# Optimization experiments

Hardware: AMD Instinct MI355X
Metric: run time of the kernel (lower is better)

## Reference

```python
import jax, jax.numpy as jnp
import numpy as np

B, N, E, H = 8, 1500, 3000, 256
HOPS = 3


def setup_inputs() -> dict:
    key = jax.random.key(0)
    ks = jax.random.split(key, 9)
    node_state = jax.random.normal(ks[0], (B, N, H), jnp.float32)
    edge_vec = jax.random.normal(ks[1], (B, E, H), jnp.float32)
    # sparse-ish 0/1 incidence matrices (avg ~3 nonzeros per row)
    node2edge = (jax.random.uniform(ks[2], (B, E, N)) < 0.002).astype(jnp.float32)
    edge2node = (jax.random.uniform(ks[3], (B, N, E)) < 0.002).astype(jnp.float32)
    s = 1.0 / np.sqrt(H).astype(np.float32)
    W_max = jax.random.uniform(ks[4], (H, H), jnp.float32, -s, s)        # linear_max, no bias
    W_fz = jax.random.uniform(ks[5], (4 * H, H), jnp.float32, -s, s)     # gated fusion
    b_fz = jnp.zeros((H,), jnp.float32)
    W_z = jax.random.uniform(ks[6], (2 * H, H), jnp.float32, -s, s)      # GRU gates, no bias
    W_r = jax.random.uniform(ks[7], (2 * H, H), jnp.float32, -s, s)
    W_t = jax.random.uniform(ks[8], (2 * H, H), jnp.float32, -s, s)
    return dict(node_state=node_state, edge_vec=edge_vec, node2edge=node2edge,
                edge2node=edge2node, W_max=W_max, W_fz=W_fz, b_fz=b_fz,
                W_z=W_z, W_r=W_r, W_t=W_t)


def _msg_pass(node_state, edge_vec, n2e, e2n):
    # n2e: (B,E,N), e2n: (B,N,E)
    edge_emb = jnp.einsum('ben,bnh->beh', n2e, node_state) + edge_vec   # (B,E,H)
    norm = jnp.sum(e2n, axis=2, keepdims=True) + 1.0                     # self-loop degree norm
    return (jnp.einsum('bne,beh->bnh', e2n, edge_emb) + node_state) / norm


def _gated_fusion(h, x, W_fz, b_fz):
    z = jax.nn.sigmoid(jnp.concatenate([h, x, h * x, h - x], -1) @ W_fz + b_fz)
    return (1.0 - z) * h + z * x


def _gru_step(h, x, W_z, W_r, W_t):
    hx = jnp.concatenate([h, x], -1)
    z = jax.nn.sigmoid(hx @ W_z)
    r = jax.nn.sigmoid(hx @ W_r)
    t = jnp.tanh(jnp.concatenate([r * h, x], -1) @ W_t)
    return (1.0 - z) * h + z * t


def reference(node_state, edge_vec, node2edge, edge2node, W_max, W_fz, b_fz, W_z, W_r, W_t):
    n2e_T = jnp.swapaxes(node2edge, 1, 2)   # (B,N,E)
    e2n_T = jnp.swapaxes(edge2node, 1, 2)   # (B,E,N)
    for _ in range(HOPS):
        bw = _msg_pass(node_state, edge_vec, node2edge, edge2node)
        fw = _msg_pass(node_state, edge_vec, e2n_T, n2e_T)
        agg = _gated_fusion(fw, bw, W_fz, b_fz)
        node_state = _gru_step(node_state, agg, W_z, W_r, W_t)
    # graph max pool: linear then max over nodes
    graph_embedding = jnp.max(node_state @ W_max, axis=1)[None]  # (1,B,H)
    return jnp.swapaxes(node_state, 0, 1), graph_embedding       # (N,B,H), (1,B,H)
```

## Files before the change

kernel.cpp:

```cpp
#include <hip/hip_runtime.h>
#include <hip/hip_bf16.h>
#include <stdint.h>

#define Bb 8
#define Nn 1500
#define Ee 3000
#define Hh 256
#define NHOPS 3
#define CAP 32
#define Mrows (Bb*Nn)
#define BE (Bb*Ee)
#define BN (Bb*Nn)

typedef __bf16 bf16x8 __attribute__((ext_vector_type(8)));
typedef float f32x4 __attribute__((ext_vector_type(4)));

__device__ __forceinline__ float sigmoidf_(float x){ return 1.f/(1.f+__expf(-x)); }

__device__ __forceinline__ unsigned short f2b(float f){
  union { float f; unsigned int u; } x; x.f = f;
  unsigned int r = (x.u + 0x7fffu + ((x.u >> 16) & 1u)) >> 16;
  return (unsigned short)r;
}
__device__ __forceinline__ float b2f(unsigned short u){
  union { unsigned int u; float f; } x; x.u = ((unsigned int)u) << 16;
  return x.f;
}
__device__ __forceinline__ ushort4 pack4(float4 v){
  return make_ushort4(f2b(v.x), f2b(v.y), f2b(v.z), f2b(v.w));
}
__device__ __forceinline__ float4 unpack4(ushort4 u){
  return make_float4(b2f(u.x), b2f(u.y), b2f(u.z), b2f(u.w));
}

#define GLL16(g, l) __builtin_amdgcn_global_load_lds( \
    (const __attribute__((address_space(1))) unsigned int*)(g), \
    (__attribute__((address_space(3))) unsigned int*)(l), 16, 0, 0)

__device__ __forceinline__ void rowscan_body(const float* __restrict__ mat, int R, int C,
                                             int* __restrict__ rowIdx, int* __restrict__ rowCnt,
                                             int* __restrict__ colIdx, int* __restrict__ colCnt,
                                             int blk) {
  int w = __builtin_amdgcn_readfirstlane((int)(threadIdx.x >> 6));
  int g = blk * 4 + w;
  if (g >= Bb * R) return;
  int b = g / R;
  int lane = threadIdx.x & 63;
  const float4* base = (const float4*)(mat + (size_t)g * C);
  int nq = C >> 2;
  int cnt = 0;
  for (int q0 = 0; q0 < nq; q0 += 64) {
    int q = q0 + lane;
    float4 v = make_float4(0.f, 0.f, 0.f, 0.f);
    if (q < nq) v = base[q];
    unsigned long long m0 = __ballot(v.x != 0.f);
    unsigned long long m1 = __ballot(v.y != 0.f);
    unsigned long long m2 = __ballot(v.z != 0.f);
    unsigned long long m3 = __ballot(v.w != 0.f);
    unsigned long long below = (1ull << lane) - 1ull;
    int myc = cnt + __popcll(m0 & below) + __popcll(m1 & below)
                  + __popcll(m2 & below) + __popcll(m3 & below);
    int c = q * 4;
    #pragma unroll
    for (int j = 0; j < 4; ++j) {
      float vv = (j == 0) ? v.x : (j == 1) ? v.y : (j == 2) ? v.z : v.w;
      if (vv != 0.f) {
        if (myc < CAP) rowIdx[(size_t)g * CAP + myc] = c + j;
        int slot = atomicAdd(&colCnt[b * C + c + j], 1);
        if (slot < CAP) colIdx[(size_t)(b * C + c + j) * CAP + slot] = g - b * R;
        ++myc;
      }
    }
    cnt += __popcll(m0) + __popcll(m1) + __popcll(m2) + __popcll(m3);
  }
  if (lane == 0) rowCnt[g] = cnt;
}

__global__ void preprocess_kernel(const float* __restrict__ n2e, const float* __restrict__ e2n,
                                  int* __restrict__ Aidx, int* __restrict__ cntA,
                                  int* __restrict__ Didx, int* __restrict__ cntD,
                                  int* __restrict__ Bidx, int* __restrict__ cntB,
                                  int* __restrict__ Cidx, int* __restrict__ cntC,
                                  const float* __restrict__ Wfz, const float* __restrict__ Wz,
                                  const float* __restrict__ Wr, const float* __restrict__ Wt,
                                  const float* __restrict__ Wmax,
                                  unsigned short* __restrict__ WfzT, unsigned short* __restrict__ WzrT,
                                  unsigned short* __restrict__ WtT, unsigned short* __restrict__ WmaxT,
                                  const float* __restrict__ in_ns, float* __restrict__ ns,
                                  const float* __restrict__ in_ev, unsigned short* __restrict__ evb) {
  int bx = blockIdx.x;
  if (bx < 6000) {
    rowscan_body(n2e, Ee, Nn, Aidx, cntA, Didx, cntD, bx);
  } else if (bx < 9000) {
    rowscan_body(e2n, Nn, Ee, Bidx, cntB, Cidx, cntC, bx - 6000);
  } else if (bx < 11560) {
    int t = (bx - 9000) * 256 + threadIdx.x;
    if (t < 196608) {
      int n = t / 768, k = t % 768;
      float v;
      if (k < 256)      v = Wfz[k * 256 + n] + Wfz[(k + 768) * 256 + n];
      else if (k < 512) v = Wfz[k * 256 + n] - Wfz[(k + 512) * 256 + n];
      else              v = Wfz[k * 256 + n];
      WfzT[t] = f2b(v);
    } else if (t < 458752) {
      int u = t - 196608;
      int j = u >> 9, k = u & 511;
      float v = (j < 256) ? Wz[k * 256 + j] : Wr[k * 256 + (j - 256)];
      WzrT[u] = f2b(v);
    } else if (t < 589824) {
      int u = t - 458752;
      int n = u >> 9, k = u & 511;
      WtT[u] = f2b(Wt[k * 256 + n]);
    } else if (t < 655360) {
      int u = t - 589824;
      int n = u >> 8, k = u & 255;
      WmaxT[u] = f2b(Wmax[k * 256 + n]);
    }
  } else if (bx < 14560) {
    int t = (bx - 11560) * 256 + threadIdx.x;
    ((float4*)ns)[t] = ((const float4*)in_ns)[t];
  } else {
    int t0 = (bx - 14560) * 1024 + threadIdx.x;
    #pragma unroll
    for (int r = 0; r < 4; ++r) {
      int t = t0 + r * 256;
      ((ushort4*)evb)[t] = pack4(((const float4*)in_ev)[t]);
    }
  }
}

__device__ __forceinline__ void sort_one(int* pp, int c) {
  if (c > CAP) c = CAP;
  int v[CAP];
  for (int j = 0; j < c; ++j) v[j] = pp[j];
  for (int j = 1; j < c; ++j) { int key = v[j]; int k = j - 1;
    while (k >= 0 && v[k] > key) { v[k+1] = v[k]; --k; } v[k+1] = key; }
  for (int j = 0; j < c; ++j) pp[j] = v[j];
}
__global__ void sort2_kernel(int* __restrict__ Cidx, const int* __restrict__ cntC,
                             int* __restrict__ Didx, const int* __restrict__ cntD) {
  int i = blockIdx.x * 256 + threadIdx.x;
  if (i < BE) sort_one(Cidx + (size_t)i * CAP, cntC[i]);
  else if (i < BE + BN) { int k = i - BE; sort_one(Didx + (size_t)k * CAP, cntD[k]); }
}

__global__ void edge_kernel(const ushort4* __restrict__ evb4, const float4* __restrict__ ns4,
                            const int* __restrict__ Aidx, const int* __restrict__ Acnt,
                            const int* __restrict__ Cidx, const int* __restrict__ Ccnt,
                            ushort4* __restrict__ eb4, ushort4* __restrict__ ef4) {
  int w = __builtin_amdgcn_readfirstlane((int)(threadIdx.x >> 6));
  int be = blockIdx.x * 4 + w;
  int lane = threadIdx.x & 63;
  int b = be / Ee;
  int cA = min(Acnt[be], CAP), cC = min(Ccnt[be], CAP);
  const int* pA = Aidx + (size_t)be * CAP;
  const int* pC = Cidx + (size_t)be * CAP;
  float4 ev = unpack4(evb4[(size_t)be * 64 + lane]);
  float4 sA = ev, sC = ev;
  for (int i = 0; i < cA; ++i) {
    int n = pA[i];
    float4 t = ns4[((size_t)b * Nn + n) * 64 + lane];
    sA.x += t.x; sA.y += t.y; sA.z += t.z; sA.w += t.w;
  }
  for (int i = 0; i < cC; ++i) {
    int n = pC[i];
    float4 t = ns4[((size_t)b * Nn + n) * 64 + lane];
    sC.x += t.x; sC.y += t.y; sC.z += t.z; sC.w += t.w;
  }
  eb4[(size_t)be * 64 + lane] = pack4(sA);
  ef4[(size_t)be * 64 + lane] = pack4(sC);
}

__global__ void node_kernel(const float4* __restrict__ ns4,
                            const ushort4* __restrict__ eb4, const ushort4* __restrict__ ef4,
                            const int* __restrict__ Bidx, const int* __restrict__ Bcnt,
                            const int* __restrict__ Didx, const int* __restrict__ Dcnt,
                            ushort4* __restrict__ Xfz4, ushort4* __restrict__ Xzr4) {
  int w = __builtin_amdgcn_readfirstlane((int)(threadIdx.x >> 6));
  int bn = blockIdx.x * 4 + w;
  int lane = threadIdx.x & 63;
  int b = bn / Nn;
  int rB = Bcnt[bn], rD = Dcnt[bn];
  int cB = min(rB, CAP), cD = min(rD, CAP);
  const int* pB = Bidx + (size_t)bn * CAP;
  const int* pD = Didx + (size_t)bn * CAP;
  float4 h0 = ns4[(size_t)bn * 64 + lane];
  float4 sb = h0, sf = h0;
  for (int i = 0; i < cB; ++i) {
    int e = pB[i];
    float4 t = unpack4(eb4[((size_t)b * Ee + e) * 64 + lane]);
    sb.x += t.x; sb.y += t.y; sb.z += t.z; sb.w += t.w;
  }
  for (int i = 0; i < cD; ++i) {
    int e = pD[i];
    float4 t = unpack4(ef4[((size_t)b * Ee + e) * 64 + lane]);
    sf.x += t.x; sf.y += t.y; sf.z += t.z; sf.w += t.w;
  }
  float ib = 1.f / (1.f + (float)rB), idf = 1.f / (1.f + (float)rD);
  sb.x *= ib; sb.y *= ib; sb.z *= ib; sb.w *= ib;
  sf.x *= idf; sf.y *= idf; sf.z *= idf; sf.w *= idf;
  float4 prod = make_float4(sf.x*sb.x, sf.y*sb.y, sf.z*sb.z, sf.w*sb.w);
  size_t m = bn;
  Xfz4[m * 192 +   0 + lane] = pack4(sf);
  Xfz4[m * 192 +  64 + lane] = pack4(sb);
  Xfz4[m * 192 + 128 + lane] = pack4(prod);
  Xzr4[m * 128 + lane] = pack4(h0);
}

#define EPI_NONE 0
#define EPI_FZ   1
#define EPI_ZR   2
#define EPI_GRU  3

template<int EPI>
__global__ __launch_bounds__(512) void gemm_kernel(
    const unsigned short* __restrict__ A, const unsigned short* __restrict__ WT,
    int M, int K,
    float* __restrict__ outf, const float* __restrict__ bfz,
    unsigned short* __restrict__ Xzr, unsigned short* __restrict__ zbuf,
    unsigned short* __restrict__ Xt, float* __restrict__ ns)
{
  __shared__ unsigned short As[128 * 64];
  __shared__ unsigned short Bs[64 * 64];
  int m0 = blockIdx.x * 128, n0 = blockIdx.y * 64;
  int tid = threadIdx.x;
  int lane = tid & 63;
  int wid = __builtin_amdgcn_readfirstlane(tid >> 6);
  int wm = wid >> 1, wn = wid & 1;
  int p = lane >> 4;
  int q = lane & 7;
  int lr = lane >> 3;
  f32x4 acc[2][2] = {};
  for (int k0 = 0; k0 < K; k0 += 64) {
    {
      int rl0 = wid * 16 + lr;
      int gm0 = m0 + rl0; if (gm0 > M - 1) gm0 = M - 1;
      GLL16(A + (size_t)gm0 * K + k0 + ((q ^ (rl0 & 7)) << 3), &As[(wid * 16) * 64]);
      int rl1 = rl0 + 8;
      int gm1 = m0 + rl1; if (gm1 > M - 1) gm1 = M - 1;
      GLL16(A + (size_t)gm1 * K + k0 + ((q ^ (rl1 & 7)) << 3), &As[(wid * 16 + 8) * 64]);
      int rb = wid * 8 + lr;
      GLL16(WT + (size_t)(n0 + rb) * K + k0 + ((q ^ (rb & 7)) << 3), &Bs[(wid * 8) * 64]);
    }
    __syncthreads();
    #pragma unroll
    for (int kk = 0; kk < 64; kk += 32) {
      int cq = (kk >> 3) + p;
      int ra0 = wm * 32 + (lane & 15);
      int ra1 = ra0 + 16;
      int rb0 = wn * 32 + (lane & 15);
      int rb1 = rb0 + 16;
      bf16x8 a0 = *(const bf16x8*)&As[ra0 * 64 + ((cq ^ (ra0 & 7)) << 3)];
      bf16x8 a1 = *(const bf16x8*)&As[ra1 * 64 + ((cq ^ (ra1 & 7)) << 3)];
      bf16x8 b0 = *(const bf16x8*)&Bs[rb0 * 64 + ((cq ^ (rb0 & 7)) << 3)];
      bf16x8 b1 = *(const bf16x8*)&Bs[rb1 * 64 + ((cq ^ (rb1 & 7)) << 3)];
      acc[0][0] = __builtin_amdgcn_mfma_f32_16x16x32_bf16(a0, b0, acc[0][0], 0, 0, 0);
      acc[0][1] = __builtin_amdgcn_mfma_f32_16x16x32_bf16(a0, b1, acc[0][1], 0, 0, 0);
      acc[1][0] = __builtin_amdgcn_mfma_f32_16x16x32_bf16(a1, b0, acc[1][0], 0, 0, 0);
      acc[1][1] = __builtin_amdgcn_mfma_f32_16x16x32_bf16(a1, b1, acc[1][1], 0, 0, 0);
    }
    __syncthreads();
  }
  #pragma unroll
  for (int mi = 0; mi < 2; ++mi)
  #pragma unroll
  for (int ni = 0; ni < 2; ++ni)
  #pragma unroll
  for (int j = 0; j < 4; ++j) {
    int m = m0 + wm * 32 + mi * 16 + p * 4 + j;
    int c = n0 + wn * 32 + ni * 16 + (lane & 15);
    if (m >= M) continue;
    float v = acc[mi][ni][j];
    if (EPI == EPI_NONE) {
      outf[(size_t)m * 256 + c] = v;
    } else if (EPI == EPI_FZ) {
      float z = sigmoidf_(v + bfz[c]);
      float fw = b2f(A[(size_t)m * K + c]);
      float bw = b2f(A[(size_t)m * K + 256 + c]);
      Xzr[(size_t)m * 512 + 256 + c] = f2b((1.f - z) * fw + z * bw);
    } else if (EPI == EPI_ZR) {
      float s = sigmoidf_(v);
      if (c < 256) {
        zbuf[(size_t)m * 256 + c] = f2b(s);
        Xt[(size_t)m * 512 + 256 + c] = A[(size_t)m * 512 + 256 + c];
      } else {
        int cz = c - 256;
        Xt[(size_t)m * 512 + cz] = f2b(s * ns[(size_t)m * 256 + cz]);
      }
    } else {
      float t = tanhf(v);
      float zz = b2f(zbuf[(size_t)m * 256 + c]);
      float h = ns[(size_t)m * 256 + c];
      ns[(size_t)m * 256 + c] = (1.f - zz) * h + zz * t;
    }
  }
}

__global__ void transpose_out_kernel(const float4* __restrict__ ns4, float4* __restrict__ out4,
                                     ushort4* __restrict__ nsb4) {
  int w = __builtin_amdgcn_readfirstlane((int)(threadIdx.x >> 6));
  int bn = blockIdx.x * 4 + w;
  int lane = threadIdx.x & 63;
  int b = bn / Nn, n = bn % Nn;
  float4 v = ns4[(size_t)bn * 64 + lane];
  out4[((size_t)n * Bb + b) * 64 + lane] = v;
  nsb4[(size_t)bn * 64 + lane] = pack4(v);
}

__global__ void maxpart_kernel(const float* __restrict__ tmp, float* __restrict__ part) {
  int bc = blockIdx.x;
  int b = bc / 12, ch = bc % 12;
  int h = threadIdx.x;
  float m = -1e30f;
  int nbase = ch * 125;
  for (int i = 0; i < 125; ++i)
    m = fmaxf(m, tmp[((size_t)b * Nn + nbase + i) * Hh + h]);
  part[(size_t)bc * Hh + h] = m;
}
__global__ void maxfin_kernel(const float* __restrict__ part, float* __restrict__ out) {
  int t = blockIdx.x * 256 + threadIdx.x;
  if (t >= Bb * Hh) return;
  int b = t / Hh, h = t % Hh;
  float m = -1e30f;
  for (int c = 0; c < 12; ++c) m = fmaxf(m, part[((size_t)b * 12 + c) * Hh + h]);
  out[(size_t)Nn * Bb * Hh + t] = m;
}

extern "C" void kernel_launch(void* const* d_in, const int* in_sizes, int n_in,
                              void* d_out, int out_size, void* d_ws, size_t ws_size,
                              hipStream_t stream) {
  const float* in_ns   = (const float*)d_in[0];
  const float* in_ev   = (const float*)d_in[1];
  const float* in_n2e  = (const float*)d_in[2];
  const float* in_e2n  = (const float*)d_in[3];
  const float* in_wmax = (const float*)d_in[4];
  const float* in_wfz  = (const float*)d_in[5];
  const float* in_bfz  = (const float*)d_in[6];
  const float* in_wz   = (const float*)d_in[7];
  const float* in_wr   = (const float*)d_in[8];
  const float* in_wt   = (const float*)d_in[9];
  float* out = (float*)d_out;

  char* base = (char*)d_ws;
  size_t off = 0;
  auto alloc = [&](size_t bytes) -> void* {
    void* r = base + off;
    off = (off + bytes + 255) & ~(size_t)255;
    return r;
  };
  int* cntC = (int*)alloc(BE * 4);
  int* cntD = (int*)alloc(BN * 4);
  int* cntA = (int*)alloc(BE * 4);
  int* Aidx = (int*)alloc((size_t)BE * CAP * 4);
  int* cntB = (int*)alloc(BN * 4);
  int* Bidx = (int*)alloc((size_t)BN * CAP * 4);
  int* Cidx = (int*)alloc((size_t)BE * CAP * 4);
  int* Didx = (int*)alloc((size_t)BN * CAP * 4);
  float* ns   = (float*)alloc((size_t)Mrows * Hh * 4);
  unsigned short* evb = (unsigned short*)alloc((size_t)BE * Hh * 2);
  unsigned short* eb = (unsigned short*)alloc((size_t)BE * Hh * 2);
  unsigned short* ef = (unsigned short*)alloc((size_t)BE * Hh * 2);
  float* gout = (float*)alloc((size_t)Mrows * 256 * 4);
  unsigned short* Xfz = (unsigned short*)alloc((size_t)Mrows * 768 * 2);
  unsigned short* Xzr = (unsigned short*)alloc((size_t)Mrows * 512 * 2);
  unsigned short* Xt  = (unsigned short*)alloc((size_t)Mrows * 512 * 2);
  unsigned short* zbuf = (unsigned short*)alloc((size_t)Mrows * 256 * 2);
  unsigned short* nsb = (unsigned short*)alloc((size_t)Mrows * 256 * 2);
  float* part = (float*)alloc((size_t)Bb * 12 * Hh * 4);
  unsigned short* WfzT  = (unsigned short*)alloc(256 * 768 * 2);
  unsigned short* WzrT  = (unsigned short*)alloc(512 * 512 * 2);
  unsigned short* WtT   = (unsigned short*)alloc(256 * 512 * 2);
  unsigned short* WmaxT = (unsigned short*)alloc(256 * 256 * 2);
  (void)ws_size; (void)in_sizes; (void)n_in; (void)out_size;

  hipMemsetAsync(cntC, 0, (BE + BN) * 4, stream);

  preprocess_kernel<<<16060, 256, 0, stream>>>(
      in_n2e, in_e2n,
      Aidx, cntA, Didx, cntD, Bidx, cntB, Cidx, cntC,
      in_wfz, in_wz, in_wr, in_wt, in_wmax,
      WfzT, WzrT, WtT, WmaxT,
      in_ns, ns, in_ev, evb);
  sort2_kernel<<<(BE + BN + 255) / 256, 256, 0, stream>>>(Cidx, cntC, Didx, cntD);

  dim3 gFZ(94, 4), gZR(94, 8), gT(94, 4);
  for (int hop = 0; hop < NHOPS; ++hop) {
    edge_kernel<<<BE / 4, 256, 0, stream>>>((const ushort4*)evb, (const float4*)ns,
        Aidx, cntA, Cidx, cntC, (ushort4*)eb, (ushort4*)ef);
    node_kernel<<<BN / 4, 256, 0, stream>>>((const float4*)ns,
        (const ushort4*)eb, (const ushort4*)ef,
        Bidx, cntB, Didx, cntD, (ushort4*)Xfz, (ushort4*)Xzr);
    gemm_kernel<EPI_FZ><<<gFZ, 512, 0, stream>>>(Xfz, WfzT, Mrows, 768,
        nullptr, in_bfz, Xzr, nullptr, nullptr, nullptr);
    gemm_kernel<EPI_ZR><<<gZR, 512, 0, stream>>>(Xzr, WzrT, Mrows, 512,
        nullptr, nullptr, nullptr, zbuf, Xt, ns);
    gemm_kernel<EPI_GRU><<<gT, 512, 0, stream>>>(Xt, WtT, Mrows, 512,
        nullptr, nullptr, nullptr, zbuf, nullptr, ns);
  }

  transpose_out_kernel<<<BN / 4, 256, 0, stream>>>((const float4*)ns, (float4*)out,
                                                   (ushort4*)nsb);
  gemm_kernel<EPI_NONE><<<gT, 512, 0, stream>>>(nsb, WmaxT, Mrows, 256,
      gout, nullptr, nullptr, nullptr, nullptr, nullptr);
  maxpart_kernel<<<Bb * 12, 256, 0, stream>>>(gout, part);
  maxfin_kernel<<<(Bb * Hh + 255) / 256, 256, 0, stream>>>(part, out);
}
```

Baseline: 437.5 us.

## Use bf16 node-state copy for edge gathers and fuse output transpose into GRU epilogue

The edge kernel now gathers node states from a bf16 shadow copy written by the GRU GEMM epilogue, which halves gather bandwidth. The initial fp32 copy of node_state is removed: hop 0 reads the input buffer directly. The last hop's GRU epilogue writes the transposed (N,B,H) output itself, so the separate transpose kernel is gone. The row scan in preprocessing now issues all its row loads up front, giving more loads in flight. The cost is lower precision in the edge sums, since edge_emb is built from bf16-rounded node states.

Measured after the change: 420.4 us. -3.9%, faster.

```diff
diff --git a/kernel.cpp b/kernel.cpp
--- a/kernel.cpp
+++ b/kernel.cpp
@@ -37,6 +37,7 @@
     (const __attribute__((address_space(1))) unsigned int*)(g), \
     (__attribute__((address_space(3))) unsigned int*)(l), 16, 0, 0)
 
+template<int NQ>
 __device__ __forceinline__ void rowscan_body(const float* __restrict__ mat, int R, int C,
                                              int* __restrict__ rowIdx, int* __restrict__ rowCnt,
                                              int* __restrict__ colIdx, int* __restrict__ colCnt,
@@ -48,22 +49,27 @@
   int lane = threadIdx.x & 63;
   const float4* base = (const float4*)(mat + (size_t)g * C);
   int nq = C >> 2;
+  float4 v[NQ];
+  #pragma unroll
+  for (int i = 0; i < NQ; ++i) {
+    int q = i * 64 + lane;
+    v[i] = make_float4(0.f, 0.f, 0.f, 0.f);
+    if (q < nq) v[i] = base[q];
+  }
   int cnt = 0;
-  for (int q0 = 0; q0 < nq; q0 += 64) {
-    int q = q0 + lane;
-    float4 v = make_float4(0.f, 0.f, 0.f, 0.f);
-    if (q < nq) v = base[q];
-    unsigned long long m0 = __ballot(v.x != 0.f);
-    unsigned long long m1 = __ballot(v.y != 0.f);
-    unsigned long long m2 = __ballot(v.z != 0.f);
-    unsigned long long m3 = __ballot(v.w != 0.f);
+  #pragma unroll
+  for (int i = 0; i < NQ; ++i) {
+    unsigned long long m0 = __ballot(v[i].x != 0.f);
+    unsigned long long m1 = __ballot(v[i].y != 0.f);
+    unsigned long long m2 = __ballot(v[i].z != 0.f);
+    unsigned long long m3 = __ballot(v[i].w != 0.f);
     unsigned long long below = (1ull << lane) - 1ull;
     int myc = cnt + __popcll(m0 & below) + __popcll(m1 & below)
                   + __popcll(m2 & below) + __popcll(m3 & below);
-    int c = q * 4;
+    int c = (i * 64 + lane) * 4;
     #pragma unroll
     for (int j = 0; j < 4; ++j) {
-      float vv = (j == 0) ? v.x : (j == 1) ? v.y : (j == 2) ? v.z : v.w;
+      float vv = (j == 0) ? v[i].x : (j == 1) ? v[i].y : (j == 2) ? v[i].z : v[i].w;
       if (vv != 0.f) {
         if (myc < CAP) rowIdx[(size_t)g * CAP + myc] = c + j;
         int slot = atomicAdd(&colCnt[b * C + c + j], 1);
@@ -86,13 +92,13 @@
                                   const float* __restrict__ Wmax,
                                   unsigned short* __restrict__ WfzT, unsigned short* __restrict__ WzrT,
                                   unsigned short* __restrict__ WtT, unsigned short* __restrict__ WmaxT,
-                                  const float* __restrict__ in_ns, float* __restrict__ ns,
+                                  const float* __restrict__ in_ns, unsigned short* __restrict__ nsb,
                                   const float* __restrict__ in_ev, unsigned short* __restrict__ evb) {
   int bx = blockIdx.x;
   if (bx < 6000) {
-    rowscan_body(n2e, Ee, Nn, Aidx, cntA, Didx, cntD, bx);
+    rowscan_body<6>(n2e, Ee, Nn, Aidx, cntA, Didx, cntD, bx);
   } else if (bx < 9000) {
-    rowscan_body(e2n, Nn, Ee, Bidx, cntB, Cidx, cntC, bx - 6000);
+    rowscan_body<12>(e2n, Nn, Ee, Bidx, cntB, Cidx, cntC, bx - 6000);
   } else if (bx < 11560) {
     int t = (bx - 9000) * 256 + threadIdx.x;
     if (t < 196608) {
@@ -116,11 +122,15 @@
       int n = u >> 8, k = u & 255;
       WmaxT[u] = f2b(Wmax[k * 256 + n]);
     }
-  } else if (bx < 14560) {
-    int t = (bx - 11560) * 256 + threadIdx.x;
-    ((float4*)ns)[t] = ((const float4*)in_ns)[t];
+  } else if (bx < 12310) {
+    int t0 = (bx - 11560) * 1024 + threadIdx.x;
+    #pragma unroll
+    for (int r = 0; r < 4; ++r) {
+      int t = t0 + r * 256;
+      ((ushort4*)nsb)[t] = pack4(((const float4*)in_ns)[t]);
+    }
   } else {
-    int t0 = (bx - 14560) * 1024 + threadIdx.x;
+    int t0 = (bx - 12310) * 1024 + threadIdx.x;
     #pragma unroll
     for (int r = 0; r < 4; ++r) {
       int t = t0 + r * 256;
@@ -144,7 +154,7 @@
   else if (i < BE + BN) { int k = i - BE; sort_one(Didx + (size_t)k * CAP, cntD[k]); }
 }
 
-__global__ void edge_kernel(const ushort4* __restrict__ evb4, const float4* __restrict__ ns4,
+__global__ void edge_kernel(const ushort4* __restrict__ evb4, const ushort4* __restrict__ nsb4,
                             const int* __restrict__ Aidx, const int* __restrict__ Acnt,
                             const int* __restrict__ Cidx, const int* __restrict__ Ccnt,
                             ushort4* __restrict__ eb4, ushort4* __restrict__ ef4) {
@@ -159,19 +169,19 @@
   float4 sA = ev, sC = ev;
   for (int i = 0; i < cA; ++i) {
     int n = pA[i];
-    float4 t = ns4[((size_t)b * Nn + n) * 64 + lane];
+    float4 t = unpack4(nsb4[((size_t)b * Nn + n) * 64 + lane]);
     sA.x += t.x; sA.y += t.y; sA.z += t.z; sA.w += t.w;
   }
   for (int i = 0; i < cC; ++i) {
     int n = pC[i];
-    float4 t = ns4[((size_t)b * Nn + n) * 64 + lane];
+    float4 t = unpack4(nsb4[((size_t)b * Nn + n) * 64 + lane]);
     sC.x += t.x; sC.y += t.y; sC.z += t.z; sC.w += t.w;
   }
   eb4[(size_t)be * 64 + lane] = pack4(sA);
   ef4[(size_t)be * 64 + lane] = pack4(sC);
 }
 
-__global__ void node_kernel(const float4* __restrict__ ns4,
+__global__ void node_kernel(const float4* __restrict__ nsin4,
                             const ushort4* __restrict__ eb4, const ushort4* __restrict__ ef4,
                             const int* __restrict__ Bidx, const int* __restrict__ Bcnt,
                             const int* __restrict__ Didx, const int* __restrict__ Dcnt,
@@ -184,7 +194,7 @@
   int cB = min(rB, CAP), cD = min(rD, CAP);
   const int* pB = Bidx + (size_t)bn * CAP;
   const int* pD = Didx + (size_t)bn * CAP;
-  float4 h0 = ns4[(size_t)bn * 64 + lane];
+  float4 h0 = nsin4[(size_t)bn * 64 + lane];
   float4 sb = h0, sf = h0;
   for (int i = 0; i < cB; ++i) {
     int e = pB[i];
@@ -212,13 +222,15 @@
 #define EPI_ZR   2
 #define EPI_GRU  3
 
-template<int EPI>
+template<int EPI, int LAST>
 __global__ __launch_bounds__(512) void gemm_kernel(
     const unsigned short* __restrict__ A, const unsigned short* __restrict__ WT,
     int M, int K,
     float* __restrict__ outf, const float* __restrict__ bfz,
     unsigned short* __restrict__ Xzr, unsigned short* __restrict__ zbuf,
-    unsigned short* __restrict__ Xt, float* __restrict__ ns)
+    unsigned short* __restrict__ Xt,
+    const float* __restrict__ nsin, float* __restrict__ nsout,
+    unsigned short* __restrict__ nsbout)
 {
   __shared__ unsigned short As[128 * 64];
   __shared__ unsigned short Bs[64 * 64];
@@ -285,26 +297,22 @@
         Xt[(size_t)m * 512 + 256 + c] = A[(size_t)m * 512 + 256 + c];
       } else {
         int cz = c - 256;
-        Xt[(size_t)m * 512 + cz] = f2b(s * ns[(size_t)m * 256 + cz]);
+        Xt[(size_t)m * 512 + cz] = f2b(s * nsin[(size_t)m * 256 + cz]);
       }
     } else {
       float t = tanhf(v);
       float zz = b2f(zbuf[(size_t)m * 256 + c]);
-      float h = ns[(size_t)m * 256 + c];
-      ns[(size_t)m * 256 + c] = (1.f - zz) * h + zz * t;
-    }
-  }
-}
-
-__global__ void transpose_out_kernel(const float4* __restrict__ ns4, float4* __restrict__ out4,
-                                     ushort4* __restrict__ nsb4) {
-  int w = __builtin_amdgcn_readfirstlane((int)(threadIdx.x >> 6));
-  int bn = blockIdx.x * 4 + w;
-  int lane = threadIdx.x & 63;
-  int b = bn / Nn, n = bn % Nn;
-  float4 v = ns4[(size_t)bn * 64 + lane];
-  out4[((size_t)n * Bb + b) * 64 + lane] = v;
-  nsb4[(size_t)bn * 64 + lane] = pack4(v);
+      float h = nsin[(size_t)m * 256 + c];
+      float nh = (1.f - zz) * h + zz * t;
+      nsbout[(size_t)m * 256 + c] = f2b(nh);
+      if (LAST) {
+        int bb = m / Nn, n = m - bb * Nn;
+        nsout[((size_t)n * Bb + bb) * 256 + c] = nh;
+      } else {
+        nsout[(size_t)m * 256 + c] = nh;
+      }
+    }
+  }
 }
 
 __global__ void maxpart_kernel(const float* __restrict__ tmp, float* __restrict__ part) {
@@ -357,6 +365,7 @@
   int* Cidx = (int*)alloc((size_t)BE * CAP * 4);
   int* Didx = (int*)alloc((size_t)BN * CAP * 4);
   float* ns   = (float*)alloc((size_t)Mrows * Hh * 4);
+  unsigned short* nsb = (unsigned short*)alloc((size_t)Mrows * Hh * 2);
   unsigned short* evb = (unsigned short*)alloc((size_t)BE * Hh * 2);
   unsigned short* eb = (unsigned short*)alloc((size_t)BE * Hh * 2);
   unsigned short* ef = (unsigned short*)alloc((size_t)BE * Hh * 2);
@@ -365,7 +374,6 @@
   unsigned short* Xzr = (unsigned short*)alloc((size_t)Mrows * 512 * 2);
   unsigned short* Xt  = (unsigned short*)alloc((size_t)Mrows * 512 * 2);
   unsigned short* zbuf = (unsigned short*)alloc((size_t)Mrows * 256 * 2);
-  unsigned short* nsb = (unsigned short*)alloc((size_t)Mrows * 256 * 2);
   float* part = (float*)alloc((size_t)Bb * 12 * Hh * 4);
   unsigned short* WfzT  = (unsigned short*)alloc(256 * 768 * 2);
   unsigned short* WzrT  = (unsigned short*)alloc(512 * 512 * 2);
@@ -375,33 +383,37 @@
 
   hipMemsetAsync(cntC, 0, (BE + BN) * 4, stream);
 
-  preprocess_kernel<<<16060, 256, 0, stream>>>(
+  preprocess_kernel<<<13810, 256, 0, stream>>>(
       in_n2e, in_e2n,
       Aidx, cntA, Didx, cntD, Bidx, cntB, Cidx, cntC,
       in_wfz, in_wz, in_wr, in_wt, in_wmax,
       WfzT, WzrT, WtT, WmaxT,
-      in_ns, ns, in_ev, evb);
+      in_ns, nsb, in_ev, evb);
   sort2_kernel<<<(BE + BN + 255) / 256, 256, 0, stream>>>(Cidx, cntC, Didx, cntD);
 
   dim3 gFZ(94, 4), gZR(94, 8), gT(94, 4);
   for (int hop = 0; hop < NHOPS; ++hop) {
-    edge_kernel<<<BE / 4, 256, 0, stream>>>((const ushort4*)evb, (const float4*)ns,
+    const float* nsin = (hop == 0) ? in_ns : ns;
+    edge_kernel<<<BE / 4, 256, 0, stream>>>((const ushort4*)evb, (const ushort4*)nsb,
         Aidx, cntA, Cidx, cntC, (ushort4*)eb, (ushort4*)ef);
-    node_kernel<<<BN / 4, 256, 0, stream>>>((const float4*)ns,
+    node_kernel<<<BN / 4, 256, 0, stream>>>((const float4*)nsin,
         (const ushort4*)eb, (const ushort4*)ef,
         Bidx, cntB, Didx, cntD, (ushort4*)Xfz, (ushort4*)Xzr);
-    gemm_kernel<EPI_FZ><<<gFZ, 512, 0, stream>>>(Xfz, WfzT, Mrows, 768,
-        nullptr, in_bfz, Xzr, nullptr, nullptr, nullptr);
-    gemm_kernel<EPI_ZR><<<gZR, 512, 0, stream>>>(Xzr, WzrT, Mrows, 512,
-        nullptr, nullptr, nullptr, zbuf, Xt, ns);
-    gemm_kernel<EPI_GRU><<<gT, 512, 0, stream>>>(Xt, WtT, Mrows, 512,
-        nullptr, nullptr, nullptr, zbuf, nullptr, ns);
-  }
-
-  transpose_out_kernel<<<BN / 4, 256, 0, stream>>>((const float4*)ns, (float4*)out,
-                                                   (ushort4*)nsb);
-  gemm_kernel<EPI_NONE><<<gT, 512, 0, stream>>>(nsb, WmaxT, Mrows, 256,
-      gout, nullptr, nullptr, nullptr, nullptr, nullptr);
+    gemm_kernel<EPI_FZ, 0><<<gFZ, 512, 0, stream>>>(Xfz, WfzT, Mrows, 768,
+        nullptr, in_bfz, Xzr, nullptr, nullptr, nullptr, nullptr, nullptr);
+    gemm_kernel<EPI_ZR, 0><<<gZR, 512, 0, stream>>>(Xzr, WzrT, Mrows, 512,
+        nullptr, nullptr, nullptr, zbuf, Xt, nsin, nullptr, nullptr);
+    if (hop < NHOPS - 1) {
+      gemm_kernel<EPI_GRU, 0><<<gT, 512, 0, stream>>>(Xt, WtT, Mrows, 512,
+          nullptr, nullptr, nullptr, zbuf, nullptr, nsin, ns, nsb);
+    } else {
+      gemm_kernel<EPI_GRU, 1><<<gT, 512, 0, stream>>>(Xt, WtT, Mrows, 512,
+          nullptr, nullptr, nullptr, zbuf, nullptr, nsin, out, nsb);
+    }
+  }
+
+  gemm_kernel<EPI_NONE, 0><<<gT, 512, 0, stream>>>(nsb, WmaxT, Mrows, 256,
+      gout, nullptr, nullptr, nullptr, nullptr, nullptr, nullptr, nullptr);
   maxpart_kernel<<<Bb * 12, 256, 0, stream>>>(gout, part);
   maxfin_kernel<<<(Bb * Hh + 255) / 256, 256, 0, stream>>>(part, out);
 }
```
